# Performance work log

Hardware: AMD Instinct MI355X
Metric: run time of the kernel (lower is better)

## Reference

```python
import jax, jax.numpy as jnp
import numpy as np

B, S, D, H, F = 8, 1024, 1024, 16, 4096
HD = D // H
SCALING = HD ** -0.5
EPS = 1e-5


def layer_norm(x, g, b):
    m = jnp.mean(x, axis=-1, keepdims=True)
    v = jnp.mean(jnp.square(x - m), axis=-1, keepdims=True)
    return (x - m) * jax.lax.rsqrt(v + EPS) * g + b


def setup_inputs() -> dict:
    key = jax.random.key(0)
    ks = jax.random.split(key, 8)
    std = 0.02
    return {
        "hidden_states": jax.random.normal(ks[0], (B, S, D), jnp.float32),
        "wq": jax.random.normal(ks[1], (D, D), jnp.float32) * std,
        "bq": jnp.zeros((D,), jnp.float32),
        "wk": jax.random.normal(ks[2], (D, D), jnp.float32) * std,
        "bk": jnp.zeros((D,), jnp.float32),
        "wv": jax.random.normal(ks[3], (D, D), jnp.float32) * std,
        "bv": jnp.zeros((D,), jnp.float32),
        "wo": jax.random.normal(ks[4], (D, D), jnp.float32) * std,
        "bo": jnp.zeros((D,), jnp.float32),
        "ln1_g": jnp.ones((D,), jnp.float32),
        "ln1_b": jnp.zeros((D,), jnp.float32),
        "fc1_w": jax.random.normal(ks[5], (F, D), jnp.float32) * std,
        "fc1_b": jnp.zeros((F,), jnp.float32),
        "fc2_w": jax.random.normal(ks[6], (D, F), jnp.float32) * std,
        "fc2_b": jnp.zeros((D,), jnp.float32),
        "ln2_g": jnp.ones((D,), jnp.float32),
        "ln2_b": jnp.zeros((D,), jnp.float32),
    }


def reference(hidden_states, wq, bq, wk, bk, wv, bv, wo, bo,
              ln1_g, ln1_b, fc1_w, fc1_b, fc2_w, fc2_b, ln2_g, ln2_b):
    hs = hidden_states
    residual = hs
    # --- manual multi-head self-attention (queries pre-scaled as in source) ---
    q = (hs @ wq.T + bq) * SCALING          # [B,S,D]
    k = hs @ wk.T + bk
    v = hs @ wv.T + bv
    q = q.reshape(B, S, H, HD).transpose(0, 2, 1, 3)  # [B,H,S,HD]
    k = k.reshape(B, S, H, HD).transpose(0, 2, 1, 3)
    v = v.reshape(B, S, H, HD).transpose(0, 2, 1, 3)
    scores = jnp.einsum("bhqd,bhkd->bhqk", q, k)      # [B,H,S,S]
    probs = jax.nn.softmax(scores, axis=-1)
    attn = jnp.einsum("bhqk,bhkd->bhqd", probs, v)    # [B,H,S,HD]
    attn = attn.transpose(0, 2, 1, 3).reshape(B, S, D)
    attn = attn @ wo.T + bo
    hs = layer_norm(residual + attn, ln1_g, ln1_b)
    # --- FFN ---
    residual = hs
    h = jax.nn.gelu(hs @ fc1_w.T + fc1_b, approximate=False)  # [B,S,F]
    h = h @ fc2_w.T + fc2_b
    hs = layer_norm(residual + h, ln2_g, ln2_b)
    return hs
```

## Files before the change

### kernel.cpp

```cpp
#include <hip/hip_runtime.h>
#include <hip/hip_bf16.h>
#include <math.h>

#define B_  8
#define S_  1024
#define D_  1024
#define H_  16
#define HD_ 64
#define F_  4096
#define NROWS_ (B_*S_)
#define SCALING_ 0.125f
#define EPS_ 1e-5f

typedef __attribute__((ext_vector_type(8))) short bf16x8;
typedef __attribute__((ext_vector_type(4))) float f32x4;
typedef __attribute__((ext_vector_type(4))) unsigned short us4;

__device__ __forceinline__ unsigned short f2bf(float f) {
    union { float f; unsigned int u; } x; x.f = f;
    unsigned int u = x.u;
    u += 0x7FFFu + ((u >> 16) & 1u);
    return (unsigned short)(u >> 16);
}

__device__ __forceinline__ unsigned int pack_bf2(float a, float b) {
    __hip_bfloat162 h = __float22bfloat162_rn(make_float2(a, b));
    union { __hip_bfloat162 h; unsigned int u; } c; c.h = h; return c.u;
}

__device__ __forceinline__ f32x4 mfma16(bf16x8 a, bf16x8 b, f32x4 c) {
    return __builtin_amdgcn_mfma_f32_16x16x32_bf16(a, b, c, 0, 0, 0);
}

__device__ __forceinline__ void async_copy16(const unsigned short* g, unsigned short* l) {
    __builtin_amdgcn_global_load_lds(
        (const __attribute__((address_space(1))) void*)g,
        (__attribute__((address_space(3))) void*)l,
        16, 0, 0);
}

__device__ __forceinline__ bf16x8 ld_swz(const unsigned short* lds, int row, int k) {
    const int kg = (k >> 3) ^ (row & 7);
    return *reinterpret_cast<const bf16x8*>(lds + row * 64 + kg * 8);
}

__global__ __launch_bounds__(256)
void cvt_kernel(const float* __restrict__ in, unsigned short* __restrict__ out, int n4) {
    int i = blockIdx.x * 256 + threadIdx.x;
    if (i >= n4) return;
    const float4 v = reinterpret_cast<const float4*>(in)[i];
    us4 o = { f2bf(v.x), f2bf(v.y), f2bf(v.z), f2bf(v.w) };
    reinterpret_cast<us4*>(out)[i] = o;
}

template<int MODE>
__global__ __launch_bounds__(256)
void gemm_bt(const unsigned short* __restrict__ A,
             const unsigned short* __restrict__ Bw,
             const float* __restrict__ bias,
             const float* __restrict__ resid,
             float* __restrict__ outf,
             unsigned short* __restrict__ outb,
             float scale, int M, int N, int K)
{
    alignas(16) __shared__ unsigned short lA[128 * 64];
    alignas(16) __shared__ unsigned short lB[128 * 64];
    const int tid  = threadIdx.x;
    const int lane = tid & 63, wave = tid >> 6;
    const int wr = wave >> 1, wc = wave & 1;
    const int l15 = lane & 15, lg = lane >> 4;
    const int brow = blockIdx.y * 128, bcol = blockIdx.x * 128;

    f32x4 acc[4][4];
#pragma unroll
    for (int m = 0; m < 4; ++m)
#pragma unroll
        for (int n = 0; n < 4; ++n) acc[m][n] = f32x4{0.f, 0.f, 0.f, 0.f};

    for (int k0 = 0; k0 < K; k0 += 64) {
#pragma unroll
        for (int j = 0; j < 4; ++j) {
            const int c   = wave * 4 + j;
            const int p   = c * 64 + lane;
            const int row = p >> 3;
            const int kg  = (p & 7) ^ (row & 7);
            async_copy16(&A [(size_t)(brow + row) * K + k0 + kg * 8], &lA[c * 512]);
            async_copy16(&Bw[(size_t)(bcol + row) * K + k0 + kg * 8], &lB[c * 512]);
        }
        __syncthreads();
#pragma unroll
        for (int kk = 0; kk < 2; ++kk) {
            bf16x8 af[4], bfr[4];
#pragma unroll
            for (int m = 0; m < 4; ++m) af[m]  = ld_swz(lA, wr * 64 + m * 16 + l15, kk * 32 + lg * 8);
#pragma unroll
            for (int n = 0; n < 4; ++n) bfr[n] = ld_swz(lB, wc * 64 + n * 16 + l15, kk * 32 + lg * 8);
#pragma unroll
            for (int m = 0; m < 4; ++m)
#pragma unroll
                for (int n = 0; n < 4; ++n)
                    acc[m][n] = mfma16(af[m], bfr[n], acc[m][n]);
        }
        __syncthreads();
    }

#pragma unroll
    for (int m = 0; m < 4; ++m) {
#pragma unroll
        for (int n = 0; n < 4; ++n) {
#pragma unroll
            for (int r = 0; r < 4; ++r) {
                const int grow = brow + wr * 64 + m * 16 + lg * 4 + r;
                const int gcol = bcol + wc * 64 + n * 16 + l15;
                float v = acc[m][n][r] + bias[gcol];
                if constexpr (MODE == 0) {
                    v *= scale;
                    const int b = grow >> 10, s = grow & 1023, h = gcol >> 6, hd = gcol & 63;
                    outb[(((size_t)b * H_ + h) * S_ + s) * HD_ + hd] = f2bf(v);
                } else if constexpr (MODE == 1) {
                    const int b = grow >> 10, s = grow & 1023, h = gcol >> 6, hd = gcol & 63;
                    outb[(((size_t)b * H_ + h) * HD_ + hd) * S_ + s] = f2bf(v);
                } else if constexpr (MODE == 2 || MODE == 4) {
                    outf[(size_t)grow * N + gcol] = v + resid[(size_t)grow * N + gcol];
                } else {
                    float g = 0.5f * v * (1.0f + erff(v * 0.70710678118654752f));
                    outb[(size_t)grow * N + gcol] = f2bf(g);
                }
            }
        }
    }
}

__global__ __launch_bounds__(256)
void attn_kernel(const unsigned short* __restrict__ qb,
                 const unsigned short* __restrict__ kb,
                 const unsigned short* __restrict__ vtb,
                 unsigned short* __restrict__ attn)
{
    alignas(16) __shared__ unsigned short lK[2][64 * 64];
    alignas(16) __shared__ unsigned short lV[2][64 * 64];
    alignas(16) __shared__ unsigned short lP[4][16 * 72];
    const int bh = blockIdx.x, qblk = blockIdx.y;
    const int tid = threadIdx.x, lane = tid & 63, wave = tid >> 6;
    const int l15 = lane & 15, lg = lane >> 4;
    const int b = bh >> 4, h = bh & 15;

    const unsigned short* Kg = kb  + (size_t)bh * S_ * HD_;
    const unsigned short* Vg = vtb + (size_t)bh * HD_ * S_;
    const unsigned short* Qg = qb  + ((size_t)bh * S_ + qblk * 64 + wave * 16) * HD_;

    bf16x8 qf0 = *reinterpret_cast<const bf16x8*>(Qg + l15 * HD_ + lg * 8);
    bf16x8 qf1 = *reinterpret_cast<const bf16x8*>(Qg + l15 * HD_ + lg * 8 + 32);

    float mr = -1e30f, lr = 0.f;
    f32x4 o[4];
#pragma unroll
    for (int m = 0; m < 4; ++m) o[m] = f32x4{0.f, 0.f, 0.f, 0.f};

#define STAGE(buf, t)                                                              \
    {                                                                              \
        _Pragma("unroll")                                                          \
        for (int j = 0; j < 2; ++j) {                                              \
            const int c   = wave * 2 + j;                      \
            const int p   = c * 64 + lane;                 \
            const int row = p >> 3;                                                \
            const int kg  = (p & 7) ^ (row & 7);                                   \
            async_copy16(&Kg[(size_t)((t) * 64 + row) * HD_ + kg * 8], &lK[buf][c * 512]); \
            async_copy16(&Vg[(size_t)row * S_ + (t) * 64 + kg * 8],    &lV[buf][c * 512]); \
        }                                                                          \
    }

    STAGE(0, 0);

    unsigned short* Pl = &lP[wave][0];

    for (int t = 0; t < 16; ++t) {
        const int cur = t & 1;
        __syncthreads();
        if (t < 15) STAGE(cur ^ 1, t + 1);

        f32x4 sf[4];
#pragma unroll
        for (int n = 0; n < 4; ++n) {
            f32x4 z = {0.f, 0.f, 0.f, 0.f};
            z     = mfma16(ld_swz(lK[cur], n * 16 + l15, lg * 8),      qf0, z);
            sf[n] = mfma16(ld_swz(lK[cur], n * 16 + l15, 32 + lg * 8), qf1, z);
        }

        float tmax = sf[0][0];
#pragma unroll
        for (int n = 0; n < 4; ++n)
#pragma unroll
            for (int r = 0; r < 4; ++r) tmax = fmaxf(tmax, sf[n][r]);
        tmax = fmaxf(tmax, __shfl_xor(tmax, 16, 64));
        tmax = fmaxf(tmax, __shfl_xor(tmax, 32, 64));
        const float mnew = fmaxf(mr, tmax);
        const float corr = __expf(mr - mnew);
        mr = mnew;

        float ps = 0.f;
        uint2 pk[4];
#pragma unroll
        for (int n = 0; n < 4; ++n) {
            float p0 = __expf(sf[n][0] - mr);
            float p1 = __expf(sf[n][1] - mr);
            float p2 = __expf(sf[n][2] - mr);
            float p3 = __expf(sf[n][3] - mr);
            ps += (p0 + p1) + (p2 + p3);
            pk[n].x = pack_bf2(p0, p1);
            pk[n].y = pack_bf2(p2, p3);
        }
        ps += __shfl_xor(ps, 16, 64);
        ps += __shfl_xor(ps, 32, 64);
        lr = lr * corr + ps;
#pragma unroll
        for (int m = 0; m < 4; ++m)
#pragma unroll
            for (int r = 0; r < 4; ++r) o[m][r] *= corr;

#pragma unroll
        for (int n = 0; n < 4; ++n)
            *reinterpret_cast<uint2*>(Pl + l15 * 72 + n * 16 + lg * 4) = pk[n];

#pragma unroll
        for (int kk = 0; kk < 2; ++kk) {
            bf16x8 pf = *reinterpret_cast<const bf16x8*>(Pl + l15 * 72 + kk * 32 + lg * 8);
#pragma unroll
            for (int m = 0; m < 4; ++m)
                o[m] = mfma16(ld_swz(lV[cur], m * 16 + l15, kk * 32 + lg * 8), pf, o[m]);
        }
    }
#undef STAGE

    const int s = qblk * 64 + wave * 16 + l15;
    const float rinv = 1.0f / lr;
#pragma unroll
    for (int m = 0; m < 4; ++m) {
        us4 w = { f2bf(o[m][0] * rinv), f2bf(o[m][1] * rinv),
                  f2bf(o[m][2] * rinv), f2bf(o[m][3] * rinv) };
        *reinterpret_cast<us4*>(attn + ((size_t)b * S_ + s) * D_ + h * HD_ + m * 16 + lg * 4) = w;
    }
}

__global__ __launch_bounds__(256)
void ln_kernel(const float* __restrict__ in, const float* __restrict__ gam,
               const float* __restrict__ bet,
               float* __restrict__ outf, unsigned short* __restrict__ outbf)
{
    const int row = blockIdx.x, t = threadIdx.x;
    const float4 v = reinterpret_cast<const float4*>(in + (size_t)row * D_)[t];
    float s  = v.x + v.y + v.z + v.w;
    float s2 = v.x * v.x + v.y * v.y + v.z * v.z + v.w * v.w;
#pragma unroll
    for (int off = 32; off > 0; off >>= 1) {
        s  += __shfl_down(s, off, 64);
        s2 += __shfl_down(s2, off, 64);
    }
    __shared__ float red[2][4];
    if ((t & 63) == 0) { red[0][t >> 6] = s; red[1][t >> 6] = s2; }
    __syncthreads();
    s  = red[0][0] + red[0][1] + red[0][2] + red[0][3];
    s2 = red[1][0] + red[1][1] + red[1][2] + red[1][3];
    const float mean = s * (1.0f / D_);
    const float rstd = rsqrtf(s2 * (1.0f / D_) - mean * mean + EPS_);
    const float4 g4 = reinterpret_cast<const float4*>(gam)[t];
    const float4 b4 = reinterpret_cast<const float4*>(bet)[t];
    float4 y;
    y.x = (v.x - mean) * rstd * g4.x + b4.x;
    y.y = (v.y - mean) * rstd * g4.y + b4.y;
    y.z = (v.z - mean) * rstd * g4.z + b4.z;
    y.w = (v.w - mean) * rstd * g4.w + b4.w;
    if (outf)  reinterpret_cast<float4*>(outf + (size_t)row * D_)[t] = y;
    if (outbf) {
        us4 o = { f2bf(y.x), f2bf(y.y), f2bf(y.z), f2bf(y.w) };
        reinterpret_cast<us4*>(outbf + (size_t)row * D_)[t] = o;
    }
}

extern "C" void kernel_launch(void* const* d_in, const int* in_sizes, int n_in,
                              void* d_out, int out_size, void* d_ws, size_t ws_size,
                              hipStream_t stream)
{
    const float* hs   = (const float*)d_in[0];
    const float* wq   = (const float*)d_in[1];
    const float* bq   = (const float*)d_in[2];
    const float* wk   = (const float*)d_in[3];
    const float* bk   = (const float*)d_in[4];
    const float* wv   = (const float*)d_in[5];
    const float* bv   = (const float*)d_in[6];
    const float* wo   = (const float*)d_in[7];
    const float* bo   = (const float*)d_in[8];
    const float* ln1g = (const float*)d_in[9];
    const float* ln1b = (const float*)d_in[10];
    const float* fc1w = (const float*)d_in[11];
    const float* fc1b = (const float*)d_in[12];
    const float* fc2w = (const float*)d_in[13];
    const float* fc2b = (const float*)d_in[14];
    const float* ln2g = (const float*)d_in[15];
    const float* ln2b = (const float*)d_in[16];
    float* out = (float*)d_out;

    char* ws = (char*)d_ws;
    const size_t MB = 1024 * 1024;
    unsigned short* hs_bf = (unsigned short*)(ws + 0);
    unsigned short* wq_bf = (unsigned short*)(ws + 16 * MB);
    unsigned short* wk_bf = (unsigned short*)(ws + 18 * MB);
    unsigned short* wv_bf = (unsigned short*)(ws + 20 * MB);
    unsigned short* wo_bf = (unsigned short*)(ws + 22 * MB);
    unsigned short* f1_bf = (unsigned short*)(ws + 24 * MB);
    unsigned short* f2_bf = (unsigned short*)(ws + 32 * MB);
    unsigned short* qbf   = (unsigned short*)(ws + 40 * MB);
    unsigned short* kbf   = (unsigned short*)(ws + 56 * MB);
    unsigned short* vtbf  = (unsigned short*)(ws + 72 * MB);
    unsigned short* attnb = (unsigned short*)(ws + 88 * MB);
    float*          tmp   = (float*)(ws + 104 * MB);
    float*          ln1f  = (float*)(ws + 136 * MB);
    unsigned short* ln1bf = (unsigned short*)(ws + 168 * MB);
    unsigned short* h_bf  = (unsigned short*)(ws + 40 * MB);

    cvt_kernel<<<8192, 256, 0, stream>>>(hs,   hs_bf, 2097152);
    cvt_kernel<<<1024, 256, 0, stream>>>(wq,   wq_bf,  262144);
    cvt_kernel<<<1024, 256, 0, stream>>>(wk,   wk_bf,  262144);
    cvt_kernel<<<1024, 256, 0, stream>>>(wv,   wv_bf,  262144);
    cvt_kernel<<<1024, 256, 0, stream>>>(wo,   wo_bf,  262144);
    cvt_kernel<<<4096, 256, 0, stream>>>(fc1w, f1_bf, 1048576);
    cvt_kernel<<<4096, 256, 0, stream>>>(fc2w, f2_bf, 1048576);

    gemm_bt<0><<<dim3(8, 64),  256, 0, stream>>>(hs_bf, wq_bf, bq, nullptr, nullptr, qbf,  SCALING_, NROWS_, D_, D_);
    gemm_bt<0><<<dim3(8, 64),  256, 0, stream>>>(hs_bf, wk_bf, bk, nullptr, nullptr, kbf,  1.0f,     NROWS_, D_, D_);
    gemm_bt<1><<<dim3(8, 64),  256, 0, stream>>>(hs_bf, wv_bf, bv, nullptr, nullptr, vtbf, 1.0f,     NROWS_, D_, D_);
    attn_kernel<<<dim3(B_ * H_, S_ / 64), 256, 0, stream>>>(qbf, kbf, vtbf, attnb);
    gemm_bt<2><<<dim3(8, 64),  256, 0, stream>>>(attnb, wo_bf, bo, hs, tmp, nullptr, 1.0f, NROWS_, D_, D_);
    ln_kernel<<<NROWS_, 256, 0, stream>>>(tmp, ln1g, ln1b, ln1f, ln1bf);
    gemm_bt<3><<<dim3(32, 64), 256, 0, stream>>>(ln1bf, f1_bf, fc1b, nullptr, nullptr, h_bf, 1.0f, NROWS_, F_, D_);
    gemm_bt<4><<<dim3(8, 64),  256, 0, stream>>>(h_bf, f2_bf, fc2b, ln1f, tmp, nullptr, 1.0f, NROWS_, D_, F_);
    ln_kernel<<<NROWS_, 256, 0, stream>>>(tmp, ln2g, ln2b, out, nullptr);
    (void)in_sizes; (void)n_in; (void)out_size; (void)ws_size;
}
```

Baseline: 565.6 us.

## Double-buffer GEMM LDS tiles, fuse weight conversions, use tanh GELU

```diff
diff --git a/kernel.cpp b/kernel.cpp
--- a/kernel.cpp
+++ b/kernel.cpp
@@ -45,12 +45,26 @@
 }
 
 __global__ __launch_bounds__(256)
-void cvt_kernel(const float* __restrict__ in, unsigned short* __restrict__ out, int n4) {
-    int i = blockIdx.x * 256 + threadIdx.x;
-    if (i >= n4) return;
-    const float4 v = reinterpret_cast<const float4*>(in)[i];
+void cvt_all(const float* __restrict__ hs, const float* __restrict__ wq,
+             const float* __restrict__ wk, const float* __restrict__ wv,
+             const float* __restrict__ wo, const float* __restrict__ f1,
+             const float* __restrict__ f2,
+             unsigned short* d_hs, unsigned short* d_wq, unsigned short* d_wk,
+             unsigned short* d_wv, unsigned short* d_wo, unsigned short* d_f1,
+             unsigned short* d_f2)
+{
+    const int gid = blockIdx.x * 256 + threadIdx.x;
+    const float* s; unsigned short* d; int off;
+    if      (gid < 2097152) { s = hs; d = d_hs; off = gid;           }
+    else if (gid < 2359296) { s = wq; d = d_wq; off = gid - 2097152; }
+    else if (gid < 2621440) { s = wk; d = d_wk; off = gid - 2359296; }
+    else if (gid < 2883584) { s = wv; d = d_wv; off = gid - 2621440; }
+    else if (gid < 3145728) { s = wo; d = d_wo; off = gid - 2883584; }
+    else if (gid < 4194304) { s = f1; d = d_f1; off = gid - 3145728; }
+    else                    { s = f2; d = d_f2; off = gid - 4194304; }
+    const float4 v = reinterpret_cast<const float4*>(s)[off];
     us4 o = { f2bf(v.x), f2bf(v.y), f2bf(v.z), f2bf(v.w) };
-    reinterpret_cast<us4*>(out)[i] = o;
+    reinterpret_cast<us4*>(d)[off] = o;
 }
 
 template<int MODE>
@@ -63,8 +77,8 @@
              unsigned short* __restrict__ outb,
              float scale, int M, int N, int K)
 {
-    alignas(16) __shared__ unsigned short lA[128 * 64];
-    alignas(16) __shared__ unsigned short lB[128 * 64];
+    alignas(16) __shared__ unsigned short lA[2][128 * 64];
+    alignas(16) __shared__ unsigned short lB[2][128 * 64];
     const int tid  = threadIdx.x;
     const int lane = tid & 63, wave = tid >> 6;
     const int wr = wave >> 1, wc = wave & 1;
@@ -77,32 +91,40 @@
 #pragma unroll
         for (int n = 0; n < 4; ++n) acc[m][n] = f32x4{0.f, 0.f, 0.f, 0.f};
 
-    for (int k0 = 0; k0 < K; k0 += 64) {
-#pragma unroll
-        for (int j = 0; j < 4; ++j) {
-            const int c   = wave * 4 + j;
-            const int p   = c * 64 + lane;
-            const int row = p >> 3;
-            const int kg  = (p & 7) ^ (row & 7);
-            async_copy16(&A [(size_t)(brow + row) * K + k0 + kg * 8], &lA[c * 512]);
-            async_copy16(&Bw[(size_t)(bcol + row) * K + k0 + kg * 8], &lB[c * 512]);
-        }
+#define GSTAGE(buf, k0)                                                            \
+    {                                                                              \
+        _Pragma("unroll")                                                          \
+        for (int j = 0; j < 4; ++j) {                                              \
+            const int c   = wave * 4 + j;                  \
+            const int p   = c * 64 + lane;                \
+            const int row = p >> 3;                                                \
+            const int kg  = (p & 7) ^ (row & 7);                                   \
+            async_copy16(&A [(size_t)(brow + row) * K + (k0) + kg * 8], &lA[buf][c * 512]); \
+            async_copy16(&Bw[(size_t)(bcol + row) * K + (k0) + kg * 8], &lB[buf][c * 512]); \
+        }                                                                          \
+    }
+
+    GSTAGE(0, 0);
+    const int nk = K >> 6;
+    for (int t = 0; t < nk; ++t) {
+        const int cur = t & 1;
         __syncthreads();
+        if (t + 1 < nk) GSTAGE(cur ^ 1, (t + 1) * 64);
 #pragma unroll
         for (int kk = 0; kk < 2; ++kk) {
             bf16x8 af[4], bfr[4];
 #pragma unroll
-            for (int m = 0; m < 4; ++m) af[m]  = ld_swz(lA, wr * 64 + m * 16 + l15, kk * 32 + lg * 8);
-#pragma unroll
-            for (int n = 0; n < 4; ++n) bfr[n] = ld_swz(lB, wc * 64 + n * 16 + l15, kk * 32 + lg * 8);
+            for (int m = 0; m < 4; ++m) af[m]  = ld_swz(lA[cur], wr * 64 + m * 16 + l15, kk * 32 + lg * 8);
+#pragma unroll
+            for (int n = 0; n < 4; ++n) bfr[n] = ld_swz(lB[cur], wc * 64 + n * 16 + l15, kk * 32 + lg * 8);
 #pragma unroll
             for (int m = 0; m < 4; ++m)
 #pragma unroll
                 for (int n = 0; n < 4; ++n)
                     acc[m][n] = mfma16(af[m], bfr[n], acc[m][n]);
         }
-        __syncthreads();
-    }
+    }
+#undef GSTAGE
 
 #pragma unroll
     for (int m = 0; m < 4; ++m) {
@@ -123,7 +145,10 @@
                 } else if constexpr (MODE == 2 || MODE == 4) {
                     outf[(size_t)grow * N + gcol] = v + resid[(size_t)grow * N + gcol];
                 } else {
-                    float g = 0.5f * v * (1.0f + erff(v * 0.70710678118654752f));
+                    const float z  = v * (0.7978845608028654f + 0.035677408136300125f * v * v);
+                    const float e  = __expf(2.0f * z);
+                    const float th = 1.0f - 2.0f / (e + 1.0f);
+                    const float g  = 0.5f * v * (1.0f + th);
                     outb[(size_t)grow * N + gcol] = f2bf(g);
                 }
             }
@@ -318,13 +343,8 @@
     unsigned short* ln1bf = (unsigned short*)(ws + 168 * MB);
     unsigned short* h_bf  = (unsigned short*)(ws + 40 * MB);
 
-    cvt_kernel<<<8192, 256, 0, stream>>>(hs,   hs_bf, 2097152);
-    cvt_kernel<<<1024, 256, 0, stream>>>(wq,   wq_bf,  262144);
-    cvt_kernel<<<1024, 256, 0, stream>>>(wk,   wk_bf,  262144);
-    cvt_kernel<<<1024, 256, 0, stream>>>(wv,   wv_bf,  262144);
-    cvt_kernel<<<1024, 256, 0, stream>>>(wo,   wo_bf,  262144);
-    cvt_kernel<<<4096, 256, 0, stream>>>(fc1w, f1_bf, 1048576);
-    cvt_kernel<<<4096, 256, 0, stream>>>(fc2w, f2_bf, 1048576);
+    cvt_all<<<20480, 256, 0, stream>>>(hs, wq, wk, wv, wo, fc1w, fc2w,
+                                       hs_bf, wq_bf, wk_bf, wv_bf, wo_bf, f1_bf, f2_bf);
 
     gemm_bt<0><<<dim3(8, 64),  256, 0, stream>>>(hs_bf, wq_bf, bq, nullptr, nullptr, qbf,  SCALING_, NROWS_, D_, D_);
     gemm_bt<0><<<dim3(8, 64),  256, 0, stream>>>(hs_bf, wk_bf, bk, nullptr, nullptr, kbf,  1.0f,     NROWS_, D_, D_);
```

New measurement: 519.6 us. 8.1% less time.
